# Kernel tuning notes

Measured on AMD Instinct MI355X. Metric: run time of the kernel, lower is better.

## Reference

```python
import jax, jax.numpy as jnp
import numpy as np

N = 8192
F_IN = 1024
F_OUT = 256
ALPHA = 0.2          # LeakyReLU negative slope
ADJ_DENSITY = 0.004  # pre-symmetrization edge probability -> avg degree ~65
NEG_INF = -9.0e15    # matches -9000000000000000.0 in the torch code


def setup_inputs() -> dict:
    key = jax.random.key(0)
    k_h, k_W, k_a, k_adj = jax.random.split(key, 4)
    h = jax.random.normal(k_h, (N, F_IN), dtype=jnp.float32)
    # xavier_uniform with gain=1.414
    lim_W = 1.414 * np.sqrt(6.0 / (F_IN + F_OUT))
    W = jax.random.uniform(k_W, (F_IN, F_OUT), dtype=jnp.float32, minval=-lim_W, maxval=lim_W)
    lim_a = 1.414 * np.sqrt(6.0 / (2 * F_OUT + 1))
    a = jax.random.uniform(k_a, (2 * F_OUT, 1), dtype=jnp.float32, minval=-lim_a, maxval=lim_a)
    # sparse symmetric 0/1 adjacency (float, like the torch code's dense adj)
    u = jax.random.uniform(k_adj, (N, N))
    m = u < ADJ_DENSITY
    adj = (m | m.T).astype(jnp.float32)
    return {"h": h, "adj": adj, "W": W, "a": a}


def reference(h, adj, W, a):
    # --- GAT attention ---
    Wh = h @ W                                   # [N, F_OUT]
    Wh1 = Wh @ a[:F_OUT]                          # [N, 1]
    Wh2 = Wh @ a[F_OUT:]                          # [N, 1]
    e = jax.nn.leaky_relu(Wh1 + Wh2.T, negative_slope=ALPHA)   # [N, N]
    attention = jax.nn.softmax(jnp.where(adj > 0, e, NEG_INF), axis=1)

    # --- per-row variable-k pruning of attention + attention@attention.T ---
    n = adj.shape[0]
    diag = jnp.eye(n, dtype=bool)
    adj_nodiag = jnp.where(diag, 0.0, adj)
    s2 = jnp.count_nonzero(adj_nodiag, axis=1)    # [N] int, variable k per row

    attention2step = attention @ attention.T      # [N, N] dense GEMM
    comb = attention + attention2step
    comb = jnp.where(diag, 0.0, comb)

    # threshold = s2[i]-th largest value of row i (np.partition(row, -k)[-k])
    sorted_desc = -jnp.sort(-comb, axis=1)        # [N, N] descending per row
    idx = jnp.maximum(s2 - 1, 0)[:, None]         # clamp for s2==0 rows
    thr = jnp.take_along_axis(sorted_desc, idx, axis=1)   # [N, 1]
    # keep values >= threshold (torch code zeros values strictly < partition);
    # rows with s2 == 0 are zeroed entirely
    pruned = jnp.where((s2[:, None] > 0) & (comb >= thr), comb, 0.0)
    adj_resize = (pruned > 0).astype(jnp.float32)

    # --- output (eval mode: dropout is identity); concat=True -> ELU ---
    h_prime = attention @ Wh                      # [N, F_OUT]
    return jax.nn.elu(h_prime), adj_resize
```

## Files before the change

kernel.cpp:

```cpp
#include <hip/hip_runtime.h>
#include <cstdint>
#include <cstddef>

#define NN 8192
#define KFIN 1024
#define KFOUT 256
#define MAXD 192
#define LRALPHA 0.2f

typedef float f32x4 __attribute__((ext_vector_type(4)));

__device__ __forceinline__ unsigned short bf16_rne(float x) {
  const unsigned u = __float_as_uint(x);
  return (unsigned short)((u + 0x7FFFu + ((u >> 16) & 1u)) >> 16);
}
__device__ __forceinline__ float bf16_to_f32(unsigned short b) {
  return __uint_as_float((unsigned)b << 16);
}

__global__ void __launch_bounds__(256) k_gemm(
    const float* __restrict__ A, const float* __restrict__ B,
    float* __restrict__ C, unsigned short* __restrict__ Cb) {
  __shared__ float As[32][65];
  __shared__ float Bs[32][65];
  const int tid = threadIdx.x;
  const int brow = blockIdx.y * 64;
  const int bcol = blockIdx.x * 64;
  const int tx = tid & 15;
  const int ty = tid >> 4;
  float acc[4][4];
#pragma unroll
  for (int i = 0; i < 4; ++i)
#pragma unroll
    for (int j = 0; j < 4; ++j) acc[i][j] = 0.0f;
  const int ar = tid >> 2;
  const int ac = (tid & 3) << 2;
  const int br = tid >> 4;
  const int bc = (tid & 15) << 2;
  for (int k0 = 0; k0 < KFIN; k0 += 32) {
    const float4 av0 =
        *reinterpret_cast<const float4*>(A + (size_t)(brow + ar) * KFIN + k0 + ac);
    const float4 av1 =
        *reinterpret_cast<const float4*>(A + (size_t)(brow + ar) * KFIN + k0 + 16 + ac);
    const float4 bv0 =
        *reinterpret_cast<const float4*>(B + (size_t)(k0 + br) * KFOUT + bcol + bc);
    const float4 bv1 =
        *reinterpret_cast<const float4*>(B + (size_t)(k0 + 16 + br) * KFOUT + bcol + bc);
    As[ac + 0][ar] = av0.x;
    As[ac + 1][ar] = av0.y;
    As[ac + 2][ar] = av0.z;
    As[ac + 3][ar] = av0.w;
    As[16 + ac + 0][ar] = av1.x;
    As[16 + ac + 1][ar] = av1.y;
    As[16 + ac + 2][ar] = av1.z;
    As[16 + ac + 3][ar] = av1.w;
    Bs[br][bc + 0] = bv0.x;
    Bs[br][bc + 1] = bv0.y;
    Bs[br][bc + 2] = bv0.z;
    Bs[br][bc + 3] = bv0.w;
    Bs[16 + br][bc + 0] = bv1.x;
    Bs[16 + br][bc + 1] = bv1.y;
    Bs[16 + br][bc + 2] = bv1.z;
    Bs[16 + br][bc + 3] = bv1.w;
    __syncthreads();
#pragma unroll
    for (int kk = 0; kk < 32; ++kk) {
      const float a0 = As[kk][ty * 4 + 0];
      const float a1 = As[kk][ty * 4 + 1];
      const float a2 = As[kk][ty * 4 + 2];
      const float a3 = As[kk][ty * 4 + 3];
      const float b0 = Bs[kk][tx * 4 + 0];
      const float b1 = Bs[kk][tx * 4 + 1];
      const float b2 = Bs[kk][tx * 4 + 2];
      const float b3 = Bs[kk][tx * 4 + 3];
      acc[0][0] += a0 * b0; acc[0][1] += a0 * b1; acc[0][2] += a0 * b2; acc[0][3] += a0 * b3;
      acc[1][0] += a1 * b0; acc[1][1] += a1 * b1; acc[1][2] += a1 * b2; acc[1][3] += a1 * b3;
      acc[2][0] += a2 * b0; acc[2][1] += a2 * b1; acc[2][2] += a2 * b2; acc[2][3] += a2 * b3;
      acc[3][0] += a3 * b0; acc[3][1] += a3 * b1; acc[3][2] += a3 * b2; acc[3][3] += a3 * b3;
    }
    __syncthreads();
  }
#pragma unroll
  for (int i = 0; i < 4; ++i) {
#pragma unroll
    for (int j = 0; j < 4; ++j) {
      const size_t idx = (size_t)(brow + ty * 4 + i) * KFOUT + bcol + tx * 4 + j;
      C[idx] = acc[i][j];
      if (Cb) Cb[idx] = bf16_rne(acc[i][j]);
    }
  }
}

__global__ void __launch_bounds__(256) k_rowdots(
    const float* __restrict__ Wh, const float* __restrict__ a,
    float* __restrict__ Wh1, float* __restrict__ Wh2) {
  const int wave = threadIdx.x >> 6;
  const int lane = threadIdx.x & 63;
  const int row = blockIdx.x * 4 + wave;
  const float4 w = *reinterpret_cast<const float4*>(Wh + (size_t)row * KFOUT + lane * 4);
  const float4 aA = *reinterpret_cast<const float4*>(a + lane * 4);
  const float4 aB = *reinterpret_cast<const float4*>(a + KFOUT + lane * 4);
  float sA = w.x * aA.x + w.y * aA.y + w.z * aA.z + w.w * aA.w;
  float sB = w.x * aB.x + w.y * aB.y + w.z * aB.z + w.w * aB.w;
  for (int o = 32; o > 0; o >>= 1) {
    sA += __shfl_xor(sA, o);
    sB += __shfl_xor(sB, o);
  }
  if (lane == 0) {
    Wh1[row] = sA;
    Wh2[row] = sB;
  }
}

__global__ void __launch_bounds__(256) k_csr_stats(
    const float* __restrict__ adj, const float* __restrict__ Wh1,
    const float* __restrict__ Wh2, int* __restrict__ nbr,
    int* __restrict__ deg, int* __restrict__ s2v,
    float2* __restrict__ mz, float* __restrict__ att,
    short* __restrict__ qb8) {
  const int wave = threadIdx.x >> 6;
  const int lane = threadIdx.x & 63;
  const int row = blockIdx.x * 4 + wave;
  const float* arow = adj + (size_t)row * NN;
  int* outp = nbr + (size_t)row * MAXD;
  int count = 0;
  int dflag = 0;
  int b[7];
  const unsigned long long below = (1ull << lane) - 1ull;
  for (int c0 = 0; c0 < NN; c0 += 256) {
    if (c0 > 0 && (c0 & 1023) == 0) b[(c0 >> 10) - 1] = count;
    const int c = c0 + lane * 4;
    const f32x4 v = __builtin_nontemporal_load(
        reinterpret_cast<const f32x4*>(arow + c));
    const unsigned long long m0 = __ballot(v[0] > 0.0f);
    const unsigned long long m1 = __ballot(v[1] > 0.0f);
    const unsigned long long m2 = __ballot(v[2] > 0.0f);
    const unsigned long long m3 = __ballot(v[3] > 0.0f);
    int pos = count + (int)(__popcll(m0 & below) + __popcll(m1 & below) +
                            __popcll(m2 & below) + __popcll(m3 & below));
    if (v[0] > 0.0f) { if (pos < MAXD) outp[pos] = c + 0; ++pos; if (c + 0 == row) dflag = 1; }
    if (v[1] > 0.0f) { if (pos < MAXD) outp[pos] = c + 1; ++pos; if (c + 1 == row) dflag = 1; }
    if (v[2] > 0.0f) { if (pos < MAXD) outp[pos] = c + 2; ++pos; if (c + 2 == row) dflag = 1; }
    if (v[3] > 0.0f) { if (pos < MAXD) outp[pos] = c + 3; ++pos; if (c + 3 == row) dflag = 1; }
    count += (int)(__popcll(m0) + __popcll(m1) + __popcll(m2) + __popcll(m3));
  }
  const int anyd = __any(dflag) ? 1 : 0;
  const int d = count < MAXD ? count : MAXD;
  if (lane == 0) {
    deg[row] = d;
    s2v[row] = count - anyd;
    short* q = qb8 + (size_t)row * 8;
#pragma unroll
    for (int w = 0; w < 7; ++w) {
      const int bw = b[w] < d ? b[w] : d;
      q[w] = (short)bw;
    }
    q[7] = (short)d;
  }
  const size_t rowbase = (size_t)row * MAXD;
  const int* cols = outp;
  const float w1 = Wh1[row];
  int c0i = 0x7fffffff, c1i = 0x7fffffff, c2i = 0x7fffffff;
  float e0 = -1e30f, e1 = -1e30f, e2 = -1e30f;
  const bool a0 = lane < d, a1 = lane + 64 < d, a2 = lane + 128 < d;
  if (a0) { c0i = cols[lane];       float x = w1 + Wh2[c0i]; e0 = x > 0.0f ? x : LRALPHA * x; }
  if (a1) { c1i = cols[lane + 64];  float x = w1 + Wh2[c1i]; e1 = x > 0.0f ? x : LRALPHA * x; }
  if (a2) { c2i = cols[lane + 128]; float x = w1 + Wh2[c2i]; e2 = x > 0.0f ? x : LRALPHA * x; }
  float mx = fmaxf(e0, fmaxf(e1, e2));
  for (int o = 32; o > 0; o >>= 1) mx = fmaxf(mx, __shfl_xor(mx, o));
  const float x0 = a0 ? expf(e0 - mx) : 0.0f;
  const float x1 = a1 ? expf(e1 - mx) : 0.0f;
  const float x2 = a2 ? expf(e2 - mx) : 0.0f;
  float sum = x0 + x1 + x2;
  for (int o = 32; o > 0; o >>= 1) sum += __shfl_xor(sum, o);
  const float Z = (d > 0) ? sum : 1.0f;
  const float invZ = 1.0f / Z;
  if (a0) att[rowbase + lane] = x0 * invZ;
  if (a1) att[rowbase + lane + 64] = x1 * invZ;
  if (a2) att[rowbase + lane + 128] = x2 * invZ;
  if (lane == 0) mz[row] = make_float2(mx, invZ);
}

__global__ void __launch_bounds__(256) k_att(
    const int* __restrict__ nbr, const int* __restrict__ deg,
    const float* __restrict__ Wh1, const float* __restrict__ Wh2,
    const float2* __restrict__ mz, const float* __restrict__ att,
    const float* __restrict__ Wh, const unsigned short* __restrict__ Whb,
    int2* __restrict__ edgesT, float* __restrict__ out0) {
  const int wave = threadIdx.x >> 6;
  const int lane = threadIdx.x & 63;
  const int row = blockIdx.x * 4 + wave;
  const int d = deg[row];
  const size_t rowbase = (size_t)row * MAXD;
  const int* cols = nbr + rowbase;
  const float w2r = Wh2[row];
  for (int t = lane; t < d; t += 64) {
    const int j = cols[t];
    float e2 = Wh1[j] + w2r;
    e2 = e2 > 0.0f ? e2 : LRALPHA * e2;
    const float2 m = mz[j];
    const float v = expf(e2 - m.x) * m.y;
    edgesT[rowbase + t] = make_int2(j, __float_as_int(v));
  }
  {
    const float* arow = att + rowbase;
    f32x4 p0 = {0, 0, 0, 0}, p1 = {0, 0, 0, 0};
    f32x4 p2 = {0, 0, 0, 0}, p3 = {0, 0, 0, 0};
    int t = 0;
    if (Whb) {
      for (; t + 3 < d; t += 4) {
        const int j0 = cols[t], j1 = cols[t + 1], j2 = cols[t + 2], j3 = cols[t + 3];
        const float w0 = arow[t], w1 = arow[t + 1], w2 = arow[t + 2], w3 = arow[t + 3];
        const ushort4 b0 = *reinterpret_cast<const ushort4*>(Whb + (size_t)j0 * KFOUT + lane * 4);
        const ushort4 b1 = *reinterpret_cast<const ushort4*>(Whb + (size_t)j1 * KFOUT + lane * 4);
        const ushort4 b2 = *reinterpret_cast<const ushort4*>(Whb + (size_t)j2 * KFOUT + lane * 4);
        const ushort4 b3 = *reinterpret_cast<const ushort4*>(Whb + (size_t)j3 * KFOUT + lane * 4);
        const f32x4 a0 = {bf16_to_f32(b0.x), bf16_to_f32(b0.y), bf16_to_f32(b0.z), bf16_to_f32(b0.w)};
        const f32x4 a1 = {bf16_to_f32(b1.x), bf16_to_f32(b1.y), bf16_to_f32(b1.z), bf16_to_f32(b1.w)};
        const f32x4 a2 = {bf16_to_f32(b2.x), bf16_to_f32(b2.y), bf16_to_f32(b2.z), bf16_to_f32(b2.w)};
        const f32x4 a3 = {bf16_to_f32(b3.x), bf16_to_f32(b3.y), bf16_to_f32(b3.z), bf16_to_f32(b3.w)};
        p0 += w0 * a0;
        p1 += w1 * a1;
        p2 += w2 * a2;
        p3 += w3 * a3;
      }
      for (; t < d; ++t) {
        const int j = cols[t];
        const float w = arow[t];
        const ushort4 b = *reinterpret_cast<const ushort4*>(Whb + (size_t)j * KFOUT + lane * 4);
        const f32x4 av = {bf16_to_f32(b.x), bf16_to_f32(b.y), bf16_to_f32(b.z), bf16_to_f32(b.w)};
        p0 += w * av;
      }
    } else {
      for (; t + 3 < d; t += 4) {
        const int j0 = cols[t], j1 = cols[t + 1], j2 = cols[t + 2], j3 = cols[t + 3];
        const float w0 = arow[t], w1 = arow[t + 1], w2 = arow[t + 2], w3 = arow[t + 3];
        const f32x4 a0 = *reinterpret_cast<const f32x4*>(Wh + (size_t)j0 * KFOUT + lane * 4);
        const f32x4 a1 = *reinterpret_cast<const f32x4*>(Wh + (size_t)j1 * KFOUT + lane * 4);
        const f32x4 a2 = *reinterpret_cast<const f32x4*>(Wh + (size_t)j2 * KFOUT + lane * 4);
        const f32x4 a3 = *reinterpret_cast<const f32x4*>(Wh + (size_t)j3 * KFOUT + lane * 4);
        p0 += w0 * a0;
        p1 += w1 * a1;
        p2 += w2 * a2;
        p3 += w3 * a3;
      }
      for (; t < d; ++t) {
        const int j = cols[t];
        const float w = arow[t];
        p0 += w * *reinterpret_cast<const f32x4*>(Wh + (size_t)j * KFOUT + lane * 4);
      }
    }
    const f32x4 r = (p0 + p1) + (p2 + p3);
    f32x4 o;
    o[0] = r[0] > 0.0f ? r[0] : expm1f(r[0]);
    o[1] = r[1] > 0.0f ? r[1] : expm1f(r[1]);
    o[2] = r[2] > 0.0f ? r[2] : expm1f(r[2]);
    o[3] = r[3] > 0.0f ? r[3] : expm1f(r[3]);
    __builtin_nontemporal_store(
        o, reinterpret_cast<f32x4*>(&out0[(size_t)row * KFOUT + lane * 4]));
  }
}

__global__ void __launch_bounds__(512) k_twostep(
    const int* __restrict__ nbr, const int* __restrict__ deg,
    const int* __restrict__ s2v, const float* __restrict__ att,
    const int2* __restrict__ edgesT, const short* __restrict__ qb8,
    float* __restrict__ out1) {
  __shared__ float comb[NN];
  __shared__ float wvals[MAXD];
  __shared__ unsigned short kcols[MAXD];
  __shared__ short sqb[MAXD][8];
  __shared__ unsigned int hist[256];
  __shared__ unsigned int scomp[512];
  __shared__ unsigned int shPrefix;
  __shared__ int shRemaining;
  __shared__ int shNc;
  const int tid = threadIdx.x;
  const int wave = tid >> 6;
  const int lane = tid & 63;
  const int row = blockIdx.x;
  const f32x4 z4 = {0.0f, 0.0f, 0.0f, 0.0f};
  for (int j = tid * 4; j < NN; j += 2048)
    *reinterpret_cast<f32x4*>(&comb[j]) = z4;
  const int d = deg[row];
  const int* cols = nbr + (size_t)row * MAXD;
  const float* arow = att + (size_t)row * MAXD;
  for (int t = tid; t < d; t += 512) {
    const int c = cols[t];
    kcols[t] = (unsigned short)c;
    wvals[t] = arow[t];
    *reinterpret_cast<int4*>(&sqb[t][0]) =
        *reinterpret_cast<const int4*>(&qb8[(size_t)c * 8]);
  }
  if (tid < 256) hist[tid] = 0u;
  if (tid == 0) shNc = 0;
  __syncthreads();
  {
    const int grp = lane >> 3;
    const int sub = lane & 7;
    for (int t0 = 0; t0 < d; t0 += 8) {
      const int t = t0 + grp;
      if (t < d) {
        const int qs = wave ? (int)sqb[t][wave - 1] : 0;
        const int qe = (int)sqb[t][wave];
        const float w = wvals[t];
        const int2* ek = edgesT + (size_t)kcols[t] * MAXD;
        for (int off = qs + sub; off < qe; off += 8) {
          const int2 e = ek[off];
          atomicAdd(&comb[e.x], w * __int_as_float(e.y));
        }
      }
    }
    const short* qr = qb8 + (size_t)row * 8;
    const int qlo = wave ? (int)qr[wave - 1] : 0;
    const int qhi = (int)qr[wave];
    for (int t = qlo + lane; t < qhi; t += 64) comb[(int)kcols[t]] += wvals[t];
    if (lane == 0 && wave == (row >> 10)) comb[row] = 0.0f;
  }
  __syncthreads();
  const int kk = s2v[row];
  const size_t obase = (size_t)row * NN;
  if (kk <= 0) {
    for (int j = tid * 4; j < NN; j += 2048)
      __builtin_nontemporal_store(z4, reinterpret_cast<f32x4*>(&out1[obase + j]));
    return;
  }
  for (int j = tid * 4; j < NN; j += 2048) {
    const f32x4 cv = *reinterpret_cast<const f32x4*>(&comb[j]);
#pragma unroll
    for (int q = 0; q < 4; ++q) {
      const unsigned int u = __float_as_uint(cv[q]);
      if (u != 0u) atomicAdd(&hist[u >> 24], 1u);
    }
  }
  __syncthreads();
  if (tid < 64) {
    const int bHi = 255 - 4 * lane;
    const unsigned int c0 = hist[bHi];
    const unsigned int c1 = hist[bHi - 1];
    const unsigned int c2 = hist[bHi - 2];
    const unsigned int c3 = hist[bHi - 3];
    const unsigned int gs = c0 + c1 + c2 + c3;
    unsigned int run2 = gs;
    for (int o = 1; o < 64; o <<= 1) {
      const unsigned int tt = __shfl_up(run2, o);
      if (lane >= o) run2 += tt;
    }
    const unsigned int pre = run2 - gs;
    const unsigned int rem = (unsigned int)kk;
    if (pre < rem && pre + gs >= rem) {
      unsigned int above;
      int digit;
      if (pre + c0 >= rem) { digit = bHi; above = pre; }
      else if (pre + c0 + c1 >= rem) { digit = bHi - 1; above = pre + c0; }
      else if (pre + c0 + c1 + c2 >= rem) { digit = bHi - 2; above = pre + c0 + c1; }
      else { digit = bHi - 3; above = pre + c0 + c1 + c2; }
      shPrefix = (unsigned)digit << 24;
      shRemaining = kk - (int)above;
    }
  }
  __syncthreads();
  const unsigned int prefix0 = shPrefix;
  const int remaining0 = shRemaining;
  const unsigned int digit0 = prefix0 >> 24;
  for (int j = tid * 4; j < NN; j += 2048) {
    const f32x4 cv = *reinterpret_cast<const f32x4*>(&comb[j]);
#pragma unroll
    for (int q = 0; q < 4; ++q) {
      const unsigned int u = __float_as_uint(cv[q]);
      if (u != 0u && (u >> 24) == digit0) {
        const int idx = atomicAdd(&shNc, 1);
        if (idx < 512) scomp[idx] = u;
      }
    }
  }
  __syncthreads();
  const int nc = shNc;
  if (nc <= 512) {
    if (wave == 0) {
      unsigned v0 = 0, v1 = 0, v2 = 0, v3 = 0, v4 = 0, v5 = 0, v6 = 0, v7 = 0;
      bool m0_ = false, m1_ = false, m2_ = false, m3_ = false;
      bool m4_ = false, m5_ = false, m6_ = false, m7_ = false;
#define LDV(I) { const int ix = lane + 64 * I; \
                 if (ix < nc) { v##I = scomp[ix]; m##I##_ = true; } }
      LDV(0) LDV(1) LDV(2) LDV(3) LDV(4) LDV(5) LDV(6) LDV(7)
#undef LDV
      unsigned prefix = prefix0;
      int remaining = remaining0;
#pragma unroll
      for (int pass = 1; pass < 4; ++pass) {
        const int shift = 24 - 8 * pass;
        const unsigned pmask = 0xFFFFFFFFu << (shift + 8);
        for (int b2 = lane; b2 < 256; b2 += 64) hist[b2] = 0u;
#define HADD(I) if (m##I##_ && (v##I & pmask) == prefix) \
                  atomicAdd(&hist[(v##I >> shift) & 255u], 1u);
        HADD(0) HADD(1) HADD(2) HADD(3) HADD(4) HADD(5) HADD(6) HADD(7)
#undef HADD
        const int bHi = 255 - 4 * lane;
        const unsigned c0 = hist[bHi];
        const unsigned c1 = hist[bHi - 1];
        const unsigned c2 = hist[bHi - 2];
        const unsigned c3 = hist[bHi - 3];
        const unsigned gs = c0 + c1 + c2 + c3;
        unsigned run2 = gs;
        for (int o = 1; o < 64; o <<= 1) {
          const unsigned tt = __shfl_up(run2, o);
          if (lane >= o) run2 += tt;
        }
        const unsigned pre = run2 - gs;
        const unsigned rem = (unsigned)remaining;
        unsigned npref = 0u;
        int nrem = 0;
        const bool hit = (pre < rem && pre + gs >= rem);
        if (hit) {
          unsigned above;
          int digit;
          if (pre + c0 >= rem) { digit = bHi; above = pre; }
          else if (pre + c0 + c1 >= rem) { digit = bHi - 1; above = pre + c0; }
          else if (pre + c0 + c1 + c2 >= rem) { digit = bHi - 2; above = pre + c0 + c1; }
          else { digit = bHi - 3; above = pre + c0 + c1 + c2; }
          npref = prefix | ((unsigned)digit << shift);
          nrem = remaining - (int)above;
        }
        const unsigned long long hm = __ballot(hit);
        const int hl = (int)__ffsll((long long)hm) - 1;
        prefix = __shfl(npref, hl);
        remaining = __shfl(nrem, hl);
      }
      if (lane == 0) shPrefix = prefix;
    }
  } else {
    unsigned prefix = prefix0;
    int remaining = remaining0;
    for (int pass = 1; pass < 4; ++pass) {
      const int shift = 24 - 8 * pass;
      const unsigned pmask = 0xFFFFFFFFu << (shift + 8);
      if (tid < 256) hist[tid] = 0u;
      __syncthreads();
      for (int j = tid * 4; j < NN; j += 2048) {
        const f32x4 cv = *reinterpret_cast<const f32x4*>(&comb[j]);
#pragma unroll
        for (int q = 0; q < 4; ++q) {
          const unsigned int u = __float_as_uint(cv[q]);
          if (u != 0u && (u & pmask) == prefix)
            atomicAdd(&hist[(u >> shift) & 255u], 1u);
        }
      }
      __syncthreads();
      if (tid < 64) {
        const int bHi = 255 - 4 * lane;
        const unsigned c0 = hist[bHi];
        const unsigned c1 = hist[bHi - 1];
        const unsigned c2 = hist[bHi - 2];
        const unsigned c3 = hist[bHi - 3];
        const unsigned gs = c0 + c1 + c2 + c3;
        unsigned run2 = gs;
        for (int o = 1; o < 64; o <<= 1) {
          const unsigned tt = __shfl_up(run2, o);
          if (lane >= o) run2 += tt;
        }
        const unsigned pre = run2 - gs;
        const unsigned rem = (unsigned)remaining;
        if (pre < rem && pre + gs >= rem) {
          unsigned above;
          int digit;
          if (pre + c0 >= rem) { digit = bHi; above = pre; }
          else if (pre + c0 + c1 >= rem) { digit = bHi - 1; above = pre + c0; }
          else if (pre + c0 + c1 + c2 >= rem) { digit = bHi - 2; above = pre + c0 + c1; }
          else { digit = bHi - 3; above = pre + c0 + c1 + c2; }
          shPrefix = prefix | ((unsigned)digit << shift);
          shRemaining = remaining - (int)above;
        }
      }
      __syncthreads();
      prefix = shPrefix;
      remaining = shRemaining;
      __syncthreads();
    }
  }
  __syncthreads();
  const float thr = __uint_as_float(shPrefix);
  for (int j = tid * 4; j < NN; j += 2048) {
    const f32x4 cv = *reinterpret_cast<const f32x4*>(&comb[j]);
    f32x4 ov;
    ov[0] = (cv[0] >= thr && cv[0] > 0.0f) ? 1.0f : 0.0f;
    ov[1] = (cv[1] >= thr && cv[1] > 0.0f) ? 1.0f : 0.0f;
    ov[2] = (cv[2] >= thr && cv[2] > 0.0f) ? 1.0f : 0.0f;
    ov[3] = (cv[3] >= thr && cv[3] > 0.0f) ? 1.0f : 0.0f;
    __builtin_nontemporal_store(ov, reinterpret_cast<f32x4*>(&out1[obase + j]));
  }
}

extern "C" void kernel_launch(void* const* d_in, const int* in_sizes, int n_in,
                              void* d_out, int out_size, void* d_ws, size_t ws_size,
                              hipStream_t stream) {
  const float* h = (const float*)d_in[0];
  const float* adj = (const float*)d_in[1];
  const float* W = (const float*)d_in[2];
  const float* a = (const float*)d_in[3];

  float* out0 = (float*)d_out;
  float* out1 = out0 + (size_t)NN * KFOUT;

  float* Wh = (float*)d_ws;
  float* Wh1 = Wh + (size_t)NN * KFOUT;
  float* Wh2 = Wh1 + NN;
  float* mrow = Wh2 + NN;
  float* Zrow = mrow + NN;
  float* att = Zrow + NN;
  float* edgesF = att + (size_t)NN * MAXD;
  int2* edgesT = (int2*)edgesF;
  int* nbr = (int*)(edgesF + (size_t)NN * MAXD * 2);
  int* deg = nbr + (size_t)NN * MAXD;
  int* s2v = deg + NN;
  short* qb8 = (short*)(s2v + NN);
  float2* mz = (float2*)(qb8 + (size_t)NN * 8);
  unsigned short* Whb = (unsigned short*)(mz + NN);
  const size_t need =
      (size_t)((char*)(Whb + (size_t)NN * KFOUT) - (char*)d_ws);
  const bool useB = ws_size >= need;
  unsigned short* WhbArg = useB ? Whb : nullptr;

  dim3 ggrid(KFOUT / 64, NN / 64);
  k_gemm<<<ggrid, 256, 0, stream>>>(h, W, Wh, WhbArg);
  k_rowdots<<<NN / 4, 256, 0, stream>>>(Wh, a, Wh1, Wh2);
  k_csr_stats<<<NN / 4, 256, 0, stream>>>(adj, Wh1, Wh2, nbr, deg, s2v, mz,
                                          att, qb8);
  k_att<<<NN / 4, 256, 0, stream>>>(nbr, deg, Wh1, Wh2, mz, att, Wh, WhbArg,
                                    edgesT, out0);
  k_twostep<<<NN, 512, 0, stream>>>(nbr, deg, s2v, att, edgesT, qb8, out1);
}
```

Before: 453.1 us.

## Process multiple rows per block in twostep kernel with prefetch of next row

k_twostep now handles 8 rows per block in a loop instead of one row per block. The next row's neighbor list, weights and quantile offsets are prefetched into registers while the current row's threshold selection runs, and comb is re-zeroed during the output pass. The aim is to amortize the block launch and shared-memory zeroing and to hide global load latency. In exchange the grid shrinks to 1024 blocks, which may lower occupancy and load balance across CUs, since comb uses 32KB of shared memory per block.

```diff
diff --git a/kernel.cpp b/kernel.cpp
--- a/kernel.cpp
+++ b/kernel.cpp
@@ -7,6 +7,7 @@
 #define KFOUT 256
 #define MAXD 192
 #define LRALPHA 0.2f
+#define RPB 8
 
 typedef float f32x4 __attribute__((ext_vector_type(4)));
 
@@ -278,216 +279,249 @@
   const int tid = threadIdx.x;
   const int wave = tid >> 6;
   const int lane = tid & 63;
-  const int row = blockIdx.x;
   const f32x4 z4 = {0.0f, 0.0f, 0.0f, 0.0f};
   for (int j = tid * 4; j < NN; j += 2048)
     *reinterpret_cast<f32x4*>(&comb[j]) = z4;
-  const int d = deg[row];
-  const int* cols = nbr + (size_t)row * MAXD;
-  const float* arow = att + (size_t)row * MAXD;
+  int row = blockIdx.x * RPB;
+  int d = deg[row];
   for (int t = tid; t < d; t += 512) {
-    const int c = cols[t];
+    const int c = nbr[(size_t)row * MAXD + t];
     kcols[t] = (unsigned short)c;
-    wvals[t] = arow[t];
+    wvals[t] = att[(size_t)row * MAXD + t];
     *reinterpret_cast<int4*>(&sqb[t][0]) =
         *reinterpret_cast<const int4*>(&qb8[(size_t)c * 8]);
   }
   if (tid < 256) hist[tid] = 0u;
   if (tid == 0) shNc = 0;
   __syncthreads();
-  {
-    const int grp = lane >> 3;
-    const int sub = lane & 7;
-    for (int t0 = 0; t0 < d; t0 += 8) {
-      const int t = t0 + grp;
-      if (t < d) {
-        const int qs = wave ? (int)sqb[t][wave - 1] : 0;
-        const int qe = (int)sqb[t][wave];
-        const float w = wvals[t];
-        const int2* ek = edgesT + (size_t)kcols[t] * MAXD;
-        for (int off = qs + sub; off < qe; off += 8) {
-          const int2 e = ek[off];
-          atomicAdd(&comb[e.x], w * __int_as_float(e.y));
-        }
-      }
-    }
-    const short* qr = qb8 + (size_t)row * 8;
-    const int qlo = wave ? (int)qr[wave - 1] : 0;
-    const int qhi = (int)qr[wave];
-    for (int t = qlo + lane; t < qhi; t += 64) comb[(int)kcols[t]] += wvals[t];
-    if (lane == 0 && wave == (row >> 10)) comb[row] = 0.0f;
-  }
-  __syncthreads();
-  const int kk = s2v[row];
-  const size_t obase = (size_t)row * NN;
-  if (kk <= 0) {
-    for (int j = tid * 4; j < NN; j += 2048)
-      __builtin_nontemporal_store(z4, reinterpret_cast<f32x4*>(&out1[obase + j]));
-    return;
-  }
-  for (int j = tid * 4; j < NN; j += 2048) {
-    const f32x4 cv = *reinterpret_cast<const f32x4*>(&comb[j]);
-#pragma unroll
-    for (int q = 0; q < 4; ++q) {
-      const unsigned int u = __float_as_uint(cv[q]);
-      if (u != 0u) atomicAdd(&hist[u >> 24], 1u);
-    }
-  }
-  __syncthreads();
-  if (tid < 64) {
-    const int bHi = 255 - 4 * lane;
-    const unsigned int c0 = hist[bHi];
-    const unsigned int c1 = hist[bHi - 1];
-    const unsigned int c2 = hist[bHi - 2];
-    const unsigned int c3 = hist[bHi - 3];
-    const unsigned int gs = c0 + c1 + c2 + c3;
-    unsigned int run2 = gs;
-    for (int o = 1; o < 64; o <<= 1) {
-      const unsigned int tt = __shfl_up(run2, o);
-      if (lane >= o) run2 += tt;
-    }
-    const unsigned int pre = run2 - gs;
-    const unsigned int rem = (unsigned int)kk;
-    if (pre < rem && pre + gs >= rem) {
-      unsigned int above;
-      int digit;
-      if (pre + c0 >= rem) { digit = bHi; above = pre; }
-      else if (pre + c0 + c1 >= rem) { digit = bHi - 1; above = pre + c0; }
-      else if (pre + c0 + c1 + c2 >= rem) { digit = bHi - 2; above = pre + c0 + c1; }
-      else { digit = bHi - 3; above = pre + c0 + c1 + c2; }
-      shPrefix = (unsigned)digit << 24;
-      shRemaining = kk - (int)above;
-    }
-  }
-  __syncthreads();
-  const unsigned int prefix0 = shPrefix;
-  const int remaining0 = shRemaining;
-  const unsigned int digit0 = prefix0 >> 24;
-  for (int j = tid * 4; j < NN; j += 2048) {
-    const f32x4 cv = *reinterpret_cast<const f32x4*>(&comb[j]);
-#pragma unroll
-    for (int q = 0; q < 4; ++q) {
-      const unsigned int u = __float_as_uint(cv[q]);
-      if (u != 0u && (u >> 24) == digit0) {
-        const int idx = atomicAdd(&shNc, 1);
-        if (idx < 512) scomp[idx] = u;
-      }
-    }
-  }
-  __syncthreads();
-  const int nc = shNc;
-  if (nc <= 512) {
-    if (wave == 0) {
-      unsigned v0 = 0, v1 = 0, v2 = 0, v3 = 0, v4 = 0, v5 = 0, v6 = 0, v7 = 0;
-      bool m0_ = false, m1_ = false, m2_ = false, m3_ = false;
-      bool m4_ = false, m5_ = false, m6_ = false, m7_ = false;
-#define LDV(I) { const int ix = lane + 64 * I; \
-                 if (ix < nc) { v##I = scomp[ix]; m##I##_ = true; } }
-      LDV(0) LDV(1) LDV(2) LDV(3) LDV(4) LDV(5) LDV(6) LDV(7)
-#undef LDV
-      unsigned prefix = prefix0;
-      int remaining = remaining0;
-#pragma unroll
-      for (int pass = 1; pass < 4; ++pass) {
-        const int shift = 24 - 8 * pass;
-        const unsigned pmask = 0xFFFFFFFFu << (shift + 8);
-        for (int b2 = lane; b2 < 256; b2 += 64) hist[b2] = 0u;
-#define HADD(I) if (m##I##_ && (v##I & pmask) == prefix) \
-                  atomicAdd(&hist[(v##I >> shift) & 255u], 1u);
-        HADD(0) HADD(1) HADD(2) HADD(3) HADD(4) HADD(5) HADD(6) HADD(7)
-#undef HADD
+  for (int r = 0; r < RPB; ++r) {
+    {
+      const int grp = lane >> 3;
+      const int sub = lane & 7;
+      for (int t0 = 0; t0 < d; t0 += 8) {
+        const int t = t0 + grp;
+        if (t < d) {
+          const int qs = wave ? (int)sqb[t][wave - 1] : 0;
+          const int qe = (int)sqb[t][wave];
+          const float w = wvals[t];
+          const int2* ek = edgesT + (size_t)kcols[t] * MAXD;
+          for (int off = qs + sub; off < qe; off += 8) {
+            const int2 e = ek[off];
+            atomicAdd(&comb[e.x], w * __int_as_float(e.y));
+          }
+        }
+      }
+      const short* qr = qb8 + (size_t)row * 8;
+      const int qlo = wave ? (int)qr[wave - 1] : 0;
+      const int qhi = (int)qr[wave];
+      for (int t = qlo + lane; t < qhi; t += 64) comb[(int)kcols[t]] += wvals[t];
+      if (lane == 0 && wave == (row >> 10)) comb[row] = 0.0f;
+    }
+    __syncthreads();
+    const int row2 = row + 1;
+    const bool haveNext = (r + 1 < RPB);
+    int d2 = 0;
+    int c2 = 0;
+    float w2 = 0.0f;
+    int4 q2 = make_int4(0, 0, 0, 0);
+    if (haveNext) {
+      d2 = deg[row2];
+      if (tid < d2) {
+        c2 = nbr[(size_t)row2 * MAXD + tid];
+        w2 = att[(size_t)row2 * MAXD + tid];
+        q2 = *reinterpret_cast<const int4*>(&qb8[(size_t)c2 * 8]);
+      }
+    }
+    const int kk = s2v[row];
+    const size_t obase = (size_t)row * NN;
+    bool emitReal = (kk > 0);
+    if (emitReal) {
+      for (int j = tid * 4; j < NN; j += 2048) {
+        const f32x4 cv = *reinterpret_cast<const f32x4*>(&comb[j]);
+#pragma unroll
+        for (int q = 0; q < 4; ++q) {
+          const unsigned int u = __float_as_uint(cv[q]);
+          if (u != 0u) atomicAdd(&hist[u >> 24], 1u);
+        }
+      }
+      __syncthreads();
+      if (tid < 64) {
         const int bHi = 255 - 4 * lane;
-        const unsigned c0 = hist[bHi];
-        const unsigned c1 = hist[bHi - 1];
-        const unsigned c2 = hist[bHi - 2];
-        const unsigned c3 = hist[bHi - 3];
-        const unsigned gs = c0 + c1 + c2 + c3;
-        unsigned run2 = gs;
+        const unsigned int c0 = hist[bHi];
+        const unsigned int c1 = hist[bHi - 1];
+        const unsigned int cc2 = hist[bHi - 2];
+        const unsigned int c3 = hist[bHi - 3];
+        const unsigned int gs = c0 + c1 + cc2 + c3;
+        unsigned int run2 = gs;
         for (int o = 1; o < 64; o <<= 1) {
-          const unsigned tt = __shfl_up(run2, o);
+          const unsigned int tt = __shfl_up(run2, o);
           if (lane >= o) run2 += tt;
         }
-        const unsigned pre = run2 - gs;
-        const unsigned rem = (unsigned)remaining;
-        unsigned npref = 0u;
-        int nrem = 0;
-        const bool hit = (pre < rem && pre + gs >= rem);
-        if (hit) {
-          unsigned above;
+        const unsigned int pre = run2 - gs;
+        const unsigned int rem = (unsigned int)kk;
+        if (pre < rem && pre + gs >= rem) {
+          unsigned int above;
           int digit;
           if (pre + c0 >= rem) { digit = bHi; above = pre; }
           else if (pre + c0 + c1 >= rem) { digit = bHi - 1; above = pre + c0; }
-          else if (pre + c0 + c1 + c2 >= rem) { digit = bHi - 2; above = pre + c0 + c1; }
-          else { digit = bHi - 3; above = pre + c0 + c1 + c2; }
-          npref = prefix | ((unsigned)digit << shift);
-          nrem = remaining - (int)above;
-        }
-        const unsigned long long hm = __ballot(hit);
-        const int hl = (int)__ffsll((long long)hm) - 1;
-        prefix = __shfl(npref, hl);
-        remaining = __shfl(nrem, hl);
-      }
-      if (lane == 0) shPrefix = prefix;
-    }
-  } else {
-    unsigned prefix = prefix0;
-    int remaining = remaining0;
-    for (int pass = 1; pass < 4; ++pass) {
-      const int shift = 24 - 8 * pass;
-      const unsigned pmask = 0xFFFFFFFFu << (shift + 8);
-      if (tid < 256) hist[tid] = 0u;
+          else if (pre + c0 + c1 + cc2 >= rem) { digit = bHi - 2; above = pre + c0 + c1; }
+          else { digit = bHi - 3; above = pre + c0 + c1 + cc2; }
+          shPrefix = (unsigned)digit << 24;
+          shRemaining = kk - (int)above;
+        }
+      }
       __syncthreads();
+      const unsigned int prefix0 = shPrefix;
+      const int remaining0 = shRemaining;
+      const unsigned int digit0 = prefix0 >> 24;
       for (int j = tid * 4; j < NN; j += 2048) {
         const f32x4 cv = *reinterpret_cast<const f32x4*>(&comb[j]);
 #pragma unroll
         for (int q = 0; q < 4; ++q) {
           const unsigned int u = __float_as_uint(cv[q]);
-          if (u != 0u && (u & pmask) == prefix)
-            atomicAdd(&hist[(u >> shift) & 255u], 1u);
+          if (u != 0u && (u >> 24) == digit0) {
+            const int idx = atomicAdd(&shNc, 1);
+            if (idx < 512) scomp[idx] = u;
+          }
         }
       }
       __syncthreads();
-      if (tid < 64) {
-        const int bHi = 255 - 4 * lane;
-        const unsigned c0 = hist[bHi];
-        const unsigned c1 = hist[bHi - 1];
-        const unsigned c2 = hist[bHi - 2];
-        const unsigned c3 = hist[bHi - 3];
-        const unsigned gs = c0 + c1 + c2 + c3;
-        unsigned run2 = gs;
-        for (int o = 1; o < 64; o <<= 1) {
-          const unsigned tt = __shfl_up(run2, o);
-          if (lane >= o) run2 += tt;
-        }
-        const unsigned pre = run2 - gs;
-        const unsigned rem = (unsigned)remaining;
-        if (pre < rem && pre + gs >= rem) {
-          unsigned above;
-          int digit;
-          if (pre + c0 >= rem) { digit = bHi; above = pre; }
-          else if (pre + c0 + c1 >= rem) { digit = bHi - 1; above = pre + c0; }
-          else if (pre + c0 + c1 + c2 >= rem) { digit = bHi - 2; above = pre + c0 + c1; }
-          else { digit = bHi - 3; above = pre + c0 + c1 + c2; }
-          shPrefix = prefix | ((unsigned)digit << shift);
-          shRemaining = remaining - (int)above;
+      const int nc = shNc;
+      if (nc <= 512) {
+        if (wave == 0) {
+          unsigned v0 = 0, v1 = 0, vv2 = 0, v3 = 0, v4 = 0, v5 = 0, v6 = 0, v7 = 0;
+          bool m0_ = false, m1_ = false, m2_ = false, m3_ = false;
+          bool m4_ = false, m5_ = false, m6_ = false, m7_ = false;
+#define LDV(V, M, I) { const int ix = lane + 64 * I; \
+                       if (ix < nc) { V = scomp[ix]; M = true; } }
+          LDV(v0, m0_, 0) LDV(v1, m1_, 1) LDV(vv2, m2_, 2) LDV(v3, m3_, 3)
+          LDV(v4, m4_, 4) LDV(v5, m5_, 5) LDV(v6, m6_, 6) LDV(v7, m7_, 7)
+#undef LDV
+          unsigned prefix = prefix0;
+          int remaining = remaining0;
+#pragma unroll
+          for (int pass = 1; pass < 4; ++pass) {
+            const int shift = 24 - 8 * pass;
+            const unsigned pmask = 0xFFFFFFFFu << (shift + 8);
+            for (int b2 = lane; b2 < 256; b2 += 64) hist[b2] = 0u;
+#define HADD(V, M) if (M && (V & pmask) == prefix) \
+                     atomicAdd(&hist[(V >> shift) & 255u], 1u);
+            HADD(v0, m0_) HADD(v1, m1_) HADD(vv2, m2_) HADD(v3, m3_)
+            HADD(v4, m4_) HADD(v5, m5_) HADD(v6, m6_) HADD(v7, m7_)
+#undef HADD
+            const int bHi = 255 - 4 * lane;
+            const unsigned c0 = hist[bHi];
+            const unsigned c1 = hist[bHi - 1];
+            const unsigned cc2 = hist[bHi - 2];
+            const unsigned c3 = hist[bHi - 3];
+            const unsigned gs = c0 + c1 + cc2 + c3;
+            unsigned run2 = gs;
+            for (int o = 1; o < 64; o <<= 1) {
+              const unsigned tt = __shfl_up(run2, o);
+              if (lane >= o) run2 += tt;
+            }
+            const unsigned pre = run2 - gs;
+            const unsigned rem = (unsigned)remaining;
+            unsigned npref = 0u;
+            int nrem = 0;
+            const bool hit = (pre < rem && pre + gs >= rem);
+            if (hit) {
+              unsigned above;
+              int digit;
+              if (pre + c0 >= rem) { digit = bHi; above = pre; }
+              else if (pre + c0 + c1 >= rem) { digit = bHi - 1; above = pre + c0; }
+              else if (pre + c0 + c1 + cc2 >= rem) { digit = bHi - 2; above = pre + c0 + c1; }
+              else { digit = bHi - 3; above = pre + c0 + c1 + cc2; }
+              npref = prefix | ((unsigned)digit << shift);
+              nrem = remaining - (int)above;
+            }
+            const unsigned long long hm = __ballot(hit);
+            const int hl = (int)__ffsll((long long)hm) - 1;
+            prefix = __shfl(npref, hl);
+            remaining = __shfl(nrem, hl);
+          }
+          if (lane == 0) shPrefix = prefix;
+        }
+      } else {
+        unsigned prefix = prefix0;
+        int remaining = remaining0;
+        for (int pass = 1; pass < 4; ++pass) {
+          const int shift = 24 - 8 * pass;
+          const unsigned pmask = 0xFFFFFFFFu << (shift + 8);
+          if (tid < 256) hist[tid] = 0u;
+          __syncthreads();
+          for (int j = tid * 4; j < NN; j += 2048) {
+            const f32x4 cv = *reinterpret_cast<const f32x4*>(&comb[j]);
+#pragma unroll
+            for (int q = 0; q < 4; ++q) {
+              const unsigned int u = __float_as_uint(cv[q]);
+              if (u != 0u && (u & pmask) == prefix)
+                atomicAdd(&hist[(u >> shift) & 255u], 1u);
+            }
+          }
+          __syncthreads();
+          if (tid < 64) {
+            const int bHi = 255 - 4 * lane;
+            const unsigned c0 = hist[bHi];
+            const unsigned c1 = hist[bHi - 1];
+            const unsigned cc2 = hist[bHi - 2];
+            const unsigned c3 = hist[bHi - 3];
+            const unsigned gs = c0 + c1 + cc2 + c3;
+            unsigned run2 = gs;
+            for (int o = 1; o < 64; o <<= 1) {
+              const unsigned tt = __shfl_up(run2, o);
+              if (lane >= o) run2 += tt;
+            }
+            const unsigned pre = run2 - gs;
+            const unsigned rem = (unsigned)remaining;
+            if (pre < rem && pre + gs >= rem) {
+              unsigned above;
+              int digit;
+              if (pre + c0 >= rem) { digit = bHi; above = pre; }
+              else if (pre + c0 + c1 >= rem) { digit = bHi - 1; above = pre + c0; }
+              else if (pre + c0 + c1 + cc2 >= rem) { digit = bHi - 2; above = pre + c0 + c1; }
+              else { digit = bHi - 3; above = pre + c0 + c1 + cc2; }
+              shPrefix = prefix | ((unsigned)digit << shift);
+              shRemaining = remaining - (int)above;
+            }
+          }
+          __syncthreads();
+          prefix = shPrefix;
+          remaining = shRemaining;
+          __syncthreads();
         }
       }
       __syncthreads();
-      prefix = shPrefix;
-      remaining = shRemaining;
-      __syncthreads();
-    }
-  }
-  __syncthreads();
-  const float thr = __uint_as_float(shPrefix);
-  for (int j = tid * 4; j < NN; j += 2048) {
-    const f32x4 cv = *reinterpret_cast<const f32x4*>(&comb[j]);
-    f32x4 ov;
-    ov[0] = (cv[0] >= thr && cv[0] > 0.0f) ? 1.0f : 0.0f;
-    ov[1] = (cv[1] >= thr && cv[1] > 0.0f) ? 1.0f : 0.0f;
-    ov[2] = (cv[2] >= thr && cv[2] > 0.0f) ? 1.0f : 0.0f;
-    ov[3] = (cv[3] >= thr && cv[3] > 0.0f) ? 1.0f : 0.0f;
-    __builtin_nontemporal_store(ov, reinterpret_cast<f32x4*>(&out1[obase + j]));
+    }
+    if (emitReal) {
+      const float thr = __uint_as_float(shPrefix);
+      for (int j = tid * 4; j < NN; j += 2048) {
+        f32x4* cp = reinterpret_cast<f32x4*>(&comb[j]);
+        const f32x4 cv = *cp;
+        f32x4 ov;
+        ov[0] = (cv[0] >= thr && cv[0] > 0.0f) ? 1.0f : 0.0f;
+        ov[1] = (cv[1] >= thr && cv[1] > 0.0f) ? 1.0f : 0.0f;
+        ov[2] = (cv[2] >= thr && cv[2] > 0.0f) ? 1.0f : 0.0f;
+        ov[3] = (cv[3] >= thr && cv[3] > 0.0f) ? 1.0f : 0.0f;
+        __builtin_nontemporal_store(ov, reinterpret_cast<f32x4*>(&out1[obase + j]));
+        *cp = z4;
+      }
+    } else {
+      for (int j = tid * 4; j < NN; j += 2048) {
+        __builtin_nontemporal_store(z4, reinterpret_cast<f32x4*>(&out1[obase + j]));
+        *reinterpret_cast<f32x4*>(&comb[j]) = z4;
+      }
+    }
+    if (tid < 256) hist[tid] = 0u;
+    if (tid == 0) shNc = 0;
+    if (haveNext && tid < d2) {
+      kcols[tid] = (unsigned short)c2;
+      wvals[tid] = w2;
+      *reinterpret_cast<int4*>(&sqb[tid][0]) = q2;
+    }
+    __syncthreads();
+    row = row2;
+    d = d2;
   }
 }
 
@@ -528,5 +562,5 @@
                                           att, qb8);
   k_att<<<NN / 4, 256, 0, stream>>>(nbr, deg, Wh1, Wh2, mz, att, Wh, WhbArg,
                                     edgesT, out0);
-  k_twostep<<<NN, 512, 0, stream>>>(nbr, deg, s2v, att, edgesT, qb8, out1);
-}
+  k_twostep<<<NN / RPB, 512, 0, stream>>>(nbr, deg, s2v, att, edgesT, qb8, out1);
+}
```

Measured after the change: 543.3 us. 1.2x slower.
